# Performance work log

Hardware: AMD Instinct MI355X
Metric: run time of the kernel (lower is better)

The kernel has to match this reference:

```python
import math
import jax, jax.numpy as jnp
import numpy as np

EPS = 1e-7
NUM_CLASSES = 13
LAMBDA_BOX, LAMBDA_OBJ, LAMBDA_CLS = 5.0, 1.0, 0.5


def setup_inputs() -> dict:
    key = jax.random.key(0)
    k0, k1, k2, kc, kcls, kox, koy, kw, kh = jax.random.split(key, 9)
    B = 32
    p0 = jax.random.normal(k0, (B, 18, 160, 160), dtype=jnp.float32)
    p1 = jax.random.normal(k1, (B, 18, 80, 80), dtype=jnp.float32)
    p2 = jax.random.normal(k2, (B, 18, 40, 40), dtype=jnp.float32)
    # Build 512 GT boxes, each in a UNIQUE cell of the coarsest (40x40) grid so the
    # scatter assignment is collision-free (matches torch's sequential loop exactly).
    N, GS = 512, 40
    cells = jax.random.permutation(kc, B * GS * GS)[:N]
    bi = cells // (GS * GS)
    rem = cells % (GS * GS)
    gj = rem // GS
    gi = rem % GS
    ox = jax.random.uniform(kox, (N,), minval=0.1, maxval=0.9)
    oy = jax.random.uniform(koy, (N,), minval=0.1, maxval=0.9)
    cx = (gi.astype(jnp.float32) + ox) / GS   # normalized 0-1
    cy = (gj.astype(jnp.float32) + oy) / GS
    w = jax.random.uniform(kw, (N,), minval=0.02, maxval=0.3)
    h = jax.random.uniform(kh, (N,), minval=0.02, maxval=0.3)
    cls = jax.random.randint(kcls, (N,), 0, NUM_CLASSES).astype(jnp.float32)
    targets = jnp.stack([bi.astype(jnp.float32), cls, cx, cy, w, h], axis=-1)
    return {"p0": p0, "p1": p1, "p2": p2, "targets": targets}


def bce_with_logits(x, t):
    # stable binary cross-entropy with logits, elementwise
    return jnp.maximum(x, 0.0) - x * t + jnp.log1p(jnp.exp(-jnp.abs(x)))


def focal_bce(pred, target, gamma=1.5, alpha=0.25):
    bce = bce_with_logits(pred, target)
    p_t = jnp.exp(-bce)
    return jnp.mean(alpha * (1.0 - p_t) ** gamma * bce)


def bbox_ciou(pred, tgt):
    # pred, tgt: (..., 4) in (cx, cy, w, h)
    pw, ph = pred[..., 2], pred[..., 3]
    tw, th = tgt[..., 2], tgt[..., 3]
    px1, px2 = pred[..., 0] - pw / 2, pred[..., 0] + pw / 2
    py1, py2 = pred[..., 1] - ph / 2, pred[..., 1] + ph / 2
    tx1, tx2 = tgt[..., 0] - tw / 2, tgt[..., 0] + tw / 2
    ty1, ty2 = tgt[..., 1] - th / 2, tgt[..., 1] + th / 2
    inter = jnp.clip(jnp.minimum(px2, tx2) - jnp.maximum(px1, tx1), 0.0) \
          * jnp.clip(jnp.minimum(py2, ty2) - jnp.maximum(py1, ty1), 0.0)
    union = pw * ph + tw * th - inter + EPS
    iou = inter / union
    ew = jnp.clip(jnp.maximum(px2, tx2) - jnp.minimum(px1, tx1), 0.0)
    eh = jnp.clip(jnp.maximum(py2, ty2) - jnp.minimum(py1, ty1), 0.0)
    c2 = ew * ew + eh * eh + EPS
    rho2 = (pred[..., 0] - tgt[..., 0]) ** 2 + (pred[..., 1] - tgt[..., 1]) ** 2
    v = (4.0 / math.pi ** 2) * (jnp.arctan(tw / (th + EPS)) - jnp.arctan(pw / (ph + EPS))) ** 2
    alpha = jax.lax.stop_gradient(v / (1.0 - iou + v + EPS))
    return iou - (rho2 / c2 + v * alpha)


def _scale_loss(pred, targets):
    # pred: (B, 5+NC, gs, gs); targets: (N, 6) [bi, cls, cx, cy, w, h] normalized
    B, C, gs, _ = pred.shape
    nc = C - 5
    bi = targets[:, 0].astype(jnp.int32)
    cls = targets[:, 1].astype(jnp.int32)
    cx, cy = targets[:, 2] * gs, targets[:, 3] * gs
    w, h = targets[:, 4] * gs, targets[:, 5] * gs
    gi = jnp.clip(jnp.floor(cx).astype(jnp.int32), 0, gs - 1)
    gj = jnp.clip(jnp.floor(cy).astype(jnp.int32), 0, gs - 1)
    obj_mask = jnp.zeros((B, gs, gs), jnp.float32).at[bi, gj, gi].set(1.0)
    tbox = jnp.zeros((B, gs, gs, 4), jnp.float32).at[bi, gj, gi].set(
        jnp.stack([cx - gi, cy - gj, w, h], axis=-1))
    tcls = jnp.zeros((B, gs, gs, nc), jnp.float32).at[bi, gj, gi, cls].set(0.95)

    p = jnp.transpose(pred, (0, 2, 3, 1))          # (B, gs, gs, C)
    p_xy = jax.nn.sigmoid(p[..., :2])
    p_wh = p[..., 2:4]
    p_obj = p[..., 4]
    p_cls = p[..., 5:]
    pbox = jnp.concatenate([p_xy, p_wh], axis=-1)  # (B, gs, gs, 4)

    iou = bbox_ciou(pbox, tbox)                    # (B, gs, gs)
    npos = jnp.sum(obj_mask)
    loss_box = jnp.sum((1.0 - iou) * obj_mask) / npos
    obj_tgt = obj_mask * jax.lax.stop_gradient(jnp.maximum(iou, 0.0))
    loss_obj = focal_bce(p_obj, obj_tgt)
    loss_cls = jnp.sum(bce_with_logits(p_cls, tcls) * obj_mask[..., None]) / (npos * nc)
    return loss_box, loss_obj, loss_cls


def reference(p0, p1, p2, targets):
    loss_box = loss_obj = loss_cls = jnp.float32(0.0)
    for pred in (p0, p1, p2):
        lb, lo, lc = _scale_loss(pred, targets)
        loss_box += lb
        loss_obj += lo
        loss_cls += lc
    total = LAMBDA_BOX * loss_box + LAMBDA_OBJ * loss_obj + LAMBDA_CLS * loss_cls
    return (total, loss_box, loss_obj, loss_cls)
```

## Files before the change

kernel.cpp:

```cpp
#include <hip/hip_runtime.h>
#include <math.h>


#define NBLK_BOX 6
#define NBLK_CLS 78
#define NBLK_TGT (NBLK_BOX + NBLK_CLS)
#define NBLK_SWEEP 525
#define NBLK_TOTAL (NBLK_TGT + NBLK_SWEEP)

namespace {
__device__ __forceinline__ float bce_logits(float x, float t) {
    return fmaxf(x, 0.0f) - x * t + log1pf(expf(-fabsf(x)));
}
__device__ __forceinline__ float focal_term(float x, float t) {
    float b = bce_logits(x, t);
    float pt = expf(-b);
    float om = fmaxf(1.0f - pt, 0.0f);
    return 0.25f * om * sqrtf(om) * b;
}
__device__ __forceinline__ float softplus_neg(float u) {
    return __logf(1.0f + __expf(u));
}
__device__ __forceinline__ float bce_fast(float x, float t) {
    return fmaxf(x, 0.0f) - x * t + softplus_neg(-fabsf(x));
}
__device__ __forceinline__ float focal0_fast(float x) {
    float b = fmaxf(x, 0.0f) + softplus_neg(-fabsf(x));
    float pt = __expf(-b);
    float om = fmaxf(1.0f - pt, 0.0f);
    return 0.25f * om * sqrtf(om) * b;
}
}

__global__ void __launch_bounds__(256) fnl_main(
    const float* __restrict__ p0, const float* __restrict__ p1,
    const float* __restrict__ p2, const float* __restrict__ tg,
    float* __restrict__ ws) {
    __shared__ float sm0[4], sm1[4];
    const float* const ps[3] = {p0, p1, p2};
    const int gss[3] = {160, 80, 40};

    float v0 = 0.0f, v1 = 0.0f;

    if (blockIdx.x < NBLK_BOX) {
        int gid = blockIdx.x * 256 + threadIdx.x;
        int s = gid >> 9;
        int t = gid & 511;

        const float bi  = tg[t * 6 + 0];
        const float cx  = tg[t * 6 + 2];
        const float cy  = tg[t * 6 + 3];
        const float w   = tg[t * 6 + 4];
        const float h   = tg[t * 6 + 5];
        const int b = (int)bi;

        const int gs = gss[s];
        const float fgs = (float)gs;
        float cxs = cx * fgs, cys = cy * fgs;
        int gi = (int)floorf(cxs); gi = min(max(gi, 0), gs - 1);
        int gj = (int)floorf(cys); gj = min(max(gj, 0), gs - 1);
        const float tx = cxs - (float)gi;
        const float ty = cys - (float)gj;
        const float tw = w * fgs;
        const float th = h * fgs;

        const int hw = gs * gs;
        const float* base = ps[s] + (size_t)b * 18 * hw + (size_t)gj * gs + gi;
        float pr0 = base[0];
        float pr1 = base[(size_t)hw];
        float pr2 = base[(size_t)2 * hw];
        float pr3 = base[(size_t)3 * hw];
        float pr4 = base[(size_t)4 * hw];

        const float px = 1.0f / (1.0f + expf(-pr0));
        const float py = 1.0f / (1.0f + expf(-pr1));
        const float pw = pr2;
        const float ph = pr3;

        const float eps = 1e-7f;
        float px1 = px - pw * 0.5f, px2 = px + pw * 0.5f;
        float py1 = py - ph * 0.5f, py2 = py + ph * 0.5f;
        float tx1 = tx - tw * 0.5f, tx2 = tx + tw * 0.5f;
        float ty1 = ty - th * 0.5f, ty2 = ty + th * 0.5f;
        float iw = fmaxf(fminf(px2, tx2) - fmaxf(px1, tx1), 0.0f);
        float ih = fmaxf(fminf(py2, ty2) - fmaxf(py1, ty1), 0.0f);
        float inter = iw * ih;
        float uni = pw * ph + tw * th - inter + eps;
        float iou = inter / uni;
        float ew = fmaxf(fmaxf(px2, tx2) - fminf(px1, tx1), 0.0f);
        float eh = fmaxf(fmaxf(py2, ty2) - fminf(py1, ty1), 0.0f);
        float c2 = ew * ew + eh * eh + eps;
        float rho2 = (px - tx) * (px - tx) + (py - ty) * (py - ty);
        const float four_over_pi2 = 0.405284734569351085775517852f;
        float dat = atanf(tw / (th + eps)) - atanf(pw / (ph + eps));
        float v = four_over_pi2 * dat * dat;
        float alpha = v / (1.0f - iou + v + eps);
        float ciou = iou - (rho2 / c2 + v * alpha);

        v0 = 1.0f - ciou;
        float tobj = fmaxf(ciou, 0.0f);
        v1 = focal_term(pr4, tobj) - focal_term(pr4, 0.0f);
    } else if (blockIdx.x < NBLK_TGT) {
        int g = (blockIdx.x - NBLK_BOX) * 256 + threadIdx.x;
        int sk = g >> 9;
        int t  = g & 511;
        int s  = sk / 13;
        int k  = sk - s * 13;

        const float bi  = tg[t * 6 + 0];
        const float clf = tg[t * 6 + 1];
        const float cx  = tg[t * 6 + 2];
        const float cy  = tg[t * 6 + 3];
        const int b = (int)bi;
        const int cls = (int)clf;

        const int gs = gss[s];
        const float fgs = (float)gs;
        int gi = (int)floorf(cx * fgs); gi = min(max(gi, 0), gs - 1);
        int gj = (int)floorf(cy * fgs); gj = min(max(gj, 0), gs - 1);

        const int hw = gs * gs;
        float x = ps[s][(size_t)b * 18 * hw + (size_t)(5 + k) * hw +
                        (size_t)gj * gs + gi];
        float tc = (k == cls) ? 0.95f : 0.0f;
        v0 = bce_fast(x, tc);
    } else {
        int chunk = blockIdx.x - NBLK_TGT;
        const float* p;
        int hw4, base4;
        if (chunk < 400)      { p = p0; hw4 = 6400; base4 = 0; }
        else if (chunk < 500) { p = p1; hw4 = 1600; base4 = 204800; }
        else                  { p = p2; hw4 = 400;  base4 = 256000; }

        int j0 = chunk * 512 + threadIdx.x - base4;
        #pragma unroll
        for (int r = 0; r < 2; ++r) {
            int idx = j0 + r * 256;
            int b = idx / hw4;
            int pos4 = idx - b * hw4;
            int hw = hw4 * 4;
            const float4* src = reinterpret_cast<const float4*>(
                p + (size_t)b * 18 * hw + (size_t)4 * hw);
            float4 x = src[pos4];
            v0 += focal0_fast(x.x) + focal0_fast(x.y) +
                  focal0_fast(x.z) + focal0_fast(x.w);
        }
    }

    for (int off = 32; off; off >>= 1) {
        v0 += __shfl_down(v0, off);
        v1 += __shfl_down(v1, off);
    }
    if ((threadIdx.x & 63) == 0) {
        sm0[threadIdx.x >> 6] = v0;
        sm1[threadIdx.x >> 6] = v1;
    }
    __syncthreads();
    if (threadIdx.x == 0) {
        ws[2 * blockIdx.x + 0] = sm0[0] + sm0[1] + sm0[2] + sm0[3];
        ws[2 * blockIdx.x + 1] = sm1[0] + sm1[1] + sm1[2] + sm1[3];
    }
}

__global__ void __launch_bounds__(256) fnl_finalize(
    const float* __restrict__ ws, float* __restrict__ out) {
    float a[12];
    #pragma unroll
    for (int j = 0; j < 12; ++j) a[j] = 0.0f;

    for (int i = threadIdx.x; i < NBLK_TOTAL; i += 256) {
        float v0 = ws[2 * i + 0];
        float v1 = ws[2 * i + 1];
        if (i < NBLK_BOX) {
            int s = i >> 1;
            a[s * 4 + 1] += v0;
            a[s * 4 + 3] += v1;
        } else if (i < NBLK_TGT) {
            int sk = (i - NBLK_BOX) >> 1;
            int s = sk / 13;
            a[s * 4 + 2] += v0;
        } else {
            int chunk = i - NBLK_TGT;
            int s = (chunk < 400) ? 0 : ((chunk < 500) ? 1 : 2);
            a[s * 4 + 0] += v0;
        }
    }

    __shared__ float red[12];
    if (threadIdx.x < 12) red[threadIdx.x] = 0.0f;
    __syncthreads();
    #pragma unroll
    for (int j = 0; j < 12; ++j) {
        float v = a[j];
        for (int off = 32; off; off >>= 1) v += __shfl_down(v, off);
        if ((threadIdx.x & 63) == 0) atomicAdd(&red[j], v);
    }
    __syncthreads();

    if (threadIdx.x == 0) {
        const float cells[3] = {819200.0f, 204800.0f, 51200.0f};
        const float npos = 512.0f;
        float lb = 0.0f, lo = 0.0f, lc = 0.0f;
        for (int s = 0; s < 3; ++s) {
            lb += red[s * 4 + 1] / npos;
            lo += (red[s * 4 + 0] + red[s * 4 + 3]) / cells[s];
            lc += red[s * 4 + 2] / (npos * 13.0f);
        }
        out[0] = 5.0f * lb + 1.0f * lo + 0.5f * lc;
        out[1] = lb;
        out[2] = lo;
        out[3] = lc;
    }
}

extern "C" void kernel_launch(void* const* d_in, const int* in_sizes, int n_in,
                              void* d_out, int out_size, void* d_ws, size_t ws_size,
                              hipStream_t stream) {
    const float* p0 = (const float*)d_in[0];
    const float* p1 = (const float*)d_in[1];
    const float* p2 = (const float*)d_in[2];
    const float* tg = (const float*)d_in[3];
    float* ws = (float*)d_ws;
    float* out = (float*)d_out;

    fnl_main<<<NBLK_TOTAL, 256, 0, stream>>>(p0, p1, p2, tg, ws);
    fnl_finalize<<<1, 256, 0, stream>>>(ws, out);
}
```

Before: 14.77 us.

## Fuse finalize into main kernel via per-block completion flags

Replaces the separate finalize launch with block 0 of the main kernel spin-waiting on per-work-block completion tags and then doing the final reduction. A small kernel that zeroes the tags runs first, so the launch count stays at two. The intent is to overlap the finalize block's launch and scheduling with the main work, at the cost of atomics, a polling loop, and reliance on forward progress of the other blocks.

```diff
diff --git a/kernel.cpp b/kernel.cpp
--- a/kernel.cpp
+++ b/kernel.cpp
@@ -6,7 +6,8 @@
 #define NBLK_CLS 78
 #define NBLK_TGT (NBLK_BOX + NBLK_CLS)
 #define NBLK_SWEEP 525
-#define NBLK_TOTAL (NBLK_TGT + NBLK_SWEEP)
+#define NWORK (NBLK_TGT + NBLK_SWEEP)
+#define TAG_OFF 2048
 
 namespace {
 __device__ __forceinline__ float bce_logits(float x, float t) {
@@ -32,18 +33,87 @@
 }
 }
 
-__global__ void __launch_bounds__(256) fnl_main(
+__global__ void fnl_zero_tags(unsigned* __restrict__ wsU) {
+    int i = threadIdx.x;
+    if (i < NWORK) wsU[TAG_OFF + i] = 0u;
+}
+
+__global__ void __launch_bounds__(256) fnl_fused(
     const float* __restrict__ p0, const float* __restrict__ p1,
     const float* __restrict__ p2, const float* __restrict__ tg,
-    float* __restrict__ ws) {
+    float* __restrict__ ws, float* __restrict__ out) {
+    unsigned* tags = reinterpret_cast<unsigned*>(ws) + TAG_OFF;
+
+    if (blockIdx.x == 0) {
+        int i0 = threadIdx.x, i1 = threadIdx.x + 256, i2 = threadIdx.x + 512;
+        bool d0 = false, d1 = (i1 >= NWORK), d2 = (i2 >= NWORK);
+        for (int it = 0; it < 1000000 && !(d0 && d1 && d2); ++it) {
+            if (!d0) d0 = (atomicAdd(&tags[i0], 0u) != 0u);
+            if (!d1) d1 = (atomicAdd(&tags[i1], 0u) != 0u);
+            if (!d2) d2 = (atomicAdd(&tags[i2], 0u) != 0u);
+            if (!(d0 && d1 && d2)) __builtin_amdgcn_s_sleep(2);
+        }
+        __syncthreads();
+
+        float a[12];
+        #pragma unroll
+        for (int j = 0; j < 12; ++j) a[j] = 0.0f;
+
+        for (int i = threadIdx.x; i < NWORK; i += 256) {
+            float v0 = atomicAdd(&ws[2 * i + 0], 0.0f);
+            float v1 = atomicAdd(&ws[2 * i + 1], 0.0f);
+            if (i < NBLK_BOX) {
+                int s = i >> 1;
+                a[s * 4 + 1] += v0;
+                a[s * 4 + 3] += v1;
+            } else if (i < NBLK_TGT) {
+                int sk = (i - NBLK_BOX) >> 1;
+                int s = sk / 13;
+                a[s * 4 + 2] += v0;
+            } else {
+                int chunk = i - NBLK_TGT;
+                int s = (chunk < 400) ? 0 : ((chunk < 500) ? 1 : 2);
+                a[s * 4 + 0] += v0;
+            }
+        }
+
+        __shared__ float red[12];
+        if (threadIdx.x < 12) red[threadIdx.x] = 0.0f;
+        __syncthreads();
+        #pragma unroll
+        for (int j = 0; j < 12; ++j) {
+            float v = a[j];
+            for (int off = 32; off; off >>= 1) v += __shfl_down(v, off);
+            if ((threadIdx.x & 63) == 0) atomicAdd(&red[j], v);
+        }
+        __syncthreads();
+
+        if (threadIdx.x == 0) {
+            const float cells[3] = {819200.0f, 204800.0f, 51200.0f};
+            const float npos = 512.0f;
+            float lb = 0.0f, lo = 0.0f, lc = 0.0f;
+            for (int s = 0; s < 3; ++s) {
+                lb += red[s * 4 + 1] / npos;
+                lo += (red[s * 4 + 0] + red[s * 4 + 3]) / cells[s];
+                lc += red[s * 4 + 2] / (npos * 13.0f);
+            }
+            out[0] = 5.0f * lb + 1.0f * lo + 0.5f * lc;
+            out[1] = lb;
+            out[2] = lo;
+            out[3] = lc;
+        }
+        return;
+    }
+
+    int wid = blockIdx.x - 1;
     __shared__ float sm0[4], sm1[4];
     const float* const ps[3] = {p0, p1, p2};
     const int gss[3] = {160, 80, 40};
 
     float v0 = 0.0f, v1 = 0.0f;
 
-    if (blockIdx.x < NBLK_BOX) {
-        int gid = blockIdx.x * 256 + threadIdx.x;
+    if (wid < NBLK_BOX) {
+        int gid = wid * 256 + threadIdx.x;
         int s = gid >> 9;
         int t = gid & 511;
 
@@ -100,8 +170,8 @@
         v0 = 1.0f - ciou;
         float tobj = fmaxf(ciou, 0.0f);
         v1 = focal_term(pr4, tobj) - focal_term(pr4, 0.0f);
-    } else if (blockIdx.x < NBLK_TGT) {
-        int g = (blockIdx.x - NBLK_BOX) * 256 + threadIdx.x;
+    } else if (wid < NBLK_TGT) {
+        int g = (wid - NBLK_BOX) * 256 + threadIdx.x;
         int sk = g >> 9;
         int t  = g & 511;
         int s  = sk / 13;
@@ -125,7 +195,7 @@
         float tc = (k == cls) ? 0.95f : 0.0f;
         v0 = bce_fast(x, tc);
     } else {
-        int chunk = blockIdx.x - NBLK_TGT;
+        int chunk = wid - NBLK_TGT;
         const float* p;
         int hw4, base4;
         if (chunk < 400)      { p = p0; hw4 = 6400; base4 = 0; }
@@ -157,59 +227,10 @@
     }
     __syncthreads();
     if (threadIdx.x == 0) {
-        ws[2 * blockIdx.x + 0] = sm0[0] + sm0[1] + sm0[2] + sm0[3];
-        ws[2 * blockIdx.x + 1] = sm1[0] + sm1[1] + sm1[2] + sm1[3];
-    }
-}
-
-__global__ void __launch_bounds__(256) fnl_finalize(
-    const float* __restrict__ ws, float* __restrict__ out) {
-    float a[12];
-    #pragma unroll
-    for (int j = 0; j < 12; ++j) a[j] = 0.0f;
-
-    for (int i = threadIdx.x; i < NBLK_TOTAL; i += 256) {
-        float v0 = ws[2 * i + 0];
-        float v1 = ws[2 * i + 1];
-        if (i < NBLK_BOX) {
-            int s = i >> 1;
-            a[s * 4 + 1] += v0;
-            a[s * 4 + 3] += v1;
-        } else if (i < NBLK_TGT) {
-            int sk = (i - NBLK_BOX) >> 1;
-            int s = sk / 13;
-            a[s * 4 + 2] += v0;
-        } else {
-            int chunk = i - NBLK_TGT;
-            int s = (chunk < 400) ? 0 : ((chunk < 500) ? 1 : 2);
-            a[s * 4 + 0] += v0;
-        }
-    }
-
-    __shared__ float red[12];
-    if (threadIdx.x < 12) red[threadIdx.x] = 0.0f;
-    __syncthreads();
-    #pragma unroll
-    for (int j = 0; j < 12; ++j) {
-        float v = a[j];
-        for (int off = 32; off; off >>= 1) v += __shfl_down(v, off);
-        if ((threadIdx.x & 63) == 0) atomicAdd(&red[j], v);
-    }
-    __syncthreads();
-
-    if (threadIdx.x == 0) {
-        const float cells[3] = {819200.0f, 204800.0f, 51200.0f};
-        const float npos = 512.0f;
-        float lb = 0.0f, lo = 0.0f, lc = 0.0f;
-        for (int s = 0; s < 3; ++s) {
-            lb += red[s * 4 + 1] / npos;
-            lo += (red[s * 4 + 0] + red[s * 4 + 3]) / cells[s];
-            lc += red[s * 4 + 2] / (npos * 13.0f);
-        }
-        out[0] = 5.0f * lb + 1.0f * lo + 0.5f * lc;
-        out[1] = lb;
-        out[2] = lo;
-        out[3] = lc;
+        atomicExch(&ws[2 * wid + 0], sm0[0] + sm0[1] + sm0[2] + sm0[3]);
+        atomicExch(&ws[2 * wid + 1], sm1[0] + sm1[1] + sm1[2] + sm1[3]);
+        asm volatile("s_waitcnt vmcnt(0)" ::: "memory");
+        atomicExch(&tags[wid], 1u);
     }
 }
 
@@ -223,6 +244,6 @@
     float* ws = (float*)d_ws;
     float* out = (float*)d_out;
 
-    fnl_main<<<NBLK_TOTAL, 256, 0, stream>>>(p0, p1, p2, tg, ws);
-    fnl_finalize<<<1, 256, 0, stream>>>(ws, out);
-}
+    fnl_zero_tags<<<1, 640, 0, stream>>>((unsigned*)d_ws);
+    fnl_fused<<<NWORK + 1, 256, 0, stream>>>(p0, p1, p2, tg, ws, out);
+}
```

New measurement: 19.33 us. +30.9%, slower.

## Fold class BCE into box blocks and enlarge objectness sweep chunks

Applied to the files above, without the earlier changes.

The class-BCE work moves from its own 78 blocks into the box blocks: each thread loads all 18 channels of its target cell and sums the 13 class terms itself. The objectness sweep for scales 0 and 1 now processes 2048 float4 per block instead of 512, cutting the grid from about 609 blocks to 156. The workspace becomes one float4 per block, so finalize can read it with a single pass and no loop. The intent is to cut block scheduling overhead and redundant target decoding, at the cost of fewer blocks for latency hiding and longer serial loads per thread in the box blocks.

```diff
diff --git a/kernel.cpp b/kernel.cpp
--- a/kernel.cpp
+++ b/kernel.cpp
@@ -3,10 +3,10 @@
 
 
 #define NBLK_BOX 6
-#define NBLK_CLS 78
-#define NBLK_TGT (NBLK_BOX + NBLK_CLS)
-#define NBLK_SWEEP 525
-#define NBLK_TOTAL (NBLK_TGT + NBLK_SWEEP)
+#define NBLK_S0 100
+#define NBLK_S1 25
+#define NBLK_S2 25
+#define NWORK (NBLK_BOX + NBLK_S0 + NBLK_S1 + NBLK_S2)
 
 namespace {
 __device__ __forceinline__ float bce_logits(float x, float t) {
@@ -35,24 +35,27 @@
 __global__ void __launch_bounds__(256) fnl_main(
     const float* __restrict__ p0, const float* __restrict__ p1,
     const float* __restrict__ p2, const float* __restrict__ tg,
-    float* __restrict__ ws) {
-    __shared__ float sm0[4], sm1[4];
-    const float* const ps[3] = {p0, p1, p2};
-    const int gss[3] = {160, 80, 40};
-
-    float v0 = 0.0f, v1 = 0.0f;
-
-    if (blockIdx.x < NBLK_BOX) {
-        int gid = blockIdx.x * 256 + threadIdx.x;
+    float4* __restrict__ ws4) {
+    __shared__ float sm0[4], sm1[4], sm2[4];
+    const int wid = blockIdx.x;
+
+    float v0 = 0.0f, v1 = 0.0f, v2 = 0.0f;
+
+    if (wid < NBLK_BOX) {
+        const float* const ps[3] = {p0, p1, p2};
+        const int gss[3] = {160, 80, 40};
+        int gid = wid * 256 + threadIdx.x;
         int s = gid >> 9;
         int t = gid & 511;
 
         const float bi  = tg[t * 6 + 0];
+        const float clf = tg[t * 6 + 1];
         const float cx  = tg[t * 6 + 2];
         const float cy  = tg[t * 6 + 3];
         const float w   = tg[t * 6 + 4];
         const float h   = tg[t * 6 + 5];
         const int b = (int)bi;
+        const int cls = (int)clf;
 
         const int gs = gss[s];
         const float fgs = (float)gs;
@@ -66,16 +69,14 @@
 
         const int hw = gs * gs;
         const float* base = ps[s] + (size_t)b * 18 * hw + (size_t)gj * gs + gi;
-        float pr0 = base[0];
-        float pr1 = base[(size_t)hw];
-        float pr2 = base[(size_t)2 * hw];
-        float pr3 = base[(size_t)3 * hw];
-        float pr4 = base[(size_t)4 * hw];
-
-        const float px = 1.0f / (1.0f + expf(-pr0));
-        const float py = 1.0f / (1.0f + expf(-pr1));
-        const float pw = pr2;
-        const float ph = pr3;
+        float pr[18];
+        #pragma unroll
+        for (int ch = 0; ch < 18; ++ch) pr[ch] = base[(size_t)ch * hw];
+
+        const float px = 1.0f / (1.0f + expf(-pr[0]));
+        const float py = 1.0f / (1.0f + expf(-pr[1]));
+        const float pw = pr[2];
+        const float ph = pr[3];
 
         const float eps = 1e-7f;
         float px1 = px - pw * 0.5f, px2 = px + pw * 0.5f;
@@ -99,42 +100,20 @@
 
         v0 = 1.0f - ciou;
         float tobj = fmaxf(ciou, 0.0f);
-        v1 = focal_term(pr4, tobj) - focal_term(pr4, 0.0f);
-    } else if (blockIdx.x < NBLK_TGT) {
-        int g = (blockIdx.x - NBLK_BOX) * 256 + threadIdx.x;
-        int sk = g >> 9;
-        int t  = g & 511;
-        int s  = sk / 13;
-        int k  = sk - s * 13;
-
-        const float bi  = tg[t * 6 + 0];
-        const float clf = tg[t * 6 + 1];
-        const float cx  = tg[t * 6 + 2];
-        const float cy  = tg[t * 6 + 3];
-        const int b = (int)bi;
-        const int cls = (int)clf;
-
-        const int gs = gss[s];
-        const float fgs = (float)gs;
-        int gi = (int)floorf(cx * fgs); gi = min(max(gi, 0), gs - 1);
-        int gj = (int)floorf(cy * fgs); gj = min(max(gj, 0), gs - 1);
-
-        const int hw = gs * gs;
-        float x = ps[s][(size_t)b * 18 * hw + (size_t)(5 + k) * hw +
-                        (size_t)gj * gs + gi];
-        float tc = (k == cls) ? 0.95f : 0.0f;
-        v0 = bce_fast(x, tc);
-    } else {
-        int chunk = blockIdx.x - NBLK_TGT;
+        v1 = focal_term(pr[4], tobj) - focal_term(pr[4], 0.0f);
+        #pragma unroll
+        for (int k = 0; k < 13; ++k) {
+            float tc = (k == cls) ? 0.95f : 0.0f;
+            v2 += bce_fast(pr[5 + k], tc);
+        }
+    } else if (wid < NBLK_BOX + NBLK_S0 + NBLK_S1) {
         const float* p;
-        int hw4, base4;
-        if (chunk < 400)      { p = p0; hw4 = 6400; base4 = 0; }
-        else if (chunk < 500) { p = p1; hw4 = 1600; base4 = 204800; }
-        else                  { p = p2; hw4 = 400;  base4 = 256000; }
-
-        int j0 = chunk * 512 + threadIdx.x - base4;
-        #pragma unroll
-        for (int r = 0; r < 2; ++r) {
+        int hw4, chunk;
+        if (wid < NBLK_BOX + NBLK_S0) { p = p0; hw4 = 6400; chunk = wid - NBLK_BOX; }
+        else                          { p = p1; hw4 = 1600; chunk = wid - NBLK_BOX - NBLK_S0; }
+        int j0 = chunk * 2048 + threadIdx.x;
+        #pragma unroll
+        for (int r = 0; r < 8; ++r) {
             int idx = j0 + r * 256;
             int b = idx / hw4;
             int pos4 = idx - b * hw4;
@@ -145,44 +124,64 @@
             v0 += focal0_fast(x.x) + focal0_fast(x.y) +
                   focal0_fast(x.z) + focal0_fast(x.w);
         }
+    } else {
+        int chunk = wid - NBLK_BOX - NBLK_S0 - NBLK_S1;
+        const int hw4 = 400, hw = 1600;
+        int j0 = chunk * 512 + threadIdx.x;
+        #pragma unroll
+        for (int r = 0; r < 2; ++r) {
+            int idx = j0 + r * 256;
+            int b = idx / hw4;
+            int pos4 = idx - b * hw4;
+            const float4* src = reinterpret_cast<const float4*>(
+                p2 + (size_t)b * 18 * hw + (size_t)4 * hw);
+            float4 x = src[pos4];
+            v0 += focal0_fast(x.x) + focal0_fast(x.y) +
+                  focal0_fast(x.z) + focal0_fast(x.w);
+        }
     }
 
     for (int off = 32; off; off >>= 1) {
         v0 += __shfl_down(v0, off);
         v1 += __shfl_down(v1, off);
+        v2 += __shfl_down(v2, off);
     }
     if ((threadIdx.x & 63) == 0) {
         sm0[threadIdx.x >> 6] = v0;
         sm1[threadIdx.x >> 6] = v1;
+        sm2[threadIdx.x >> 6] = v2;
     }
     __syncthreads();
     if (threadIdx.x == 0) {
-        ws[2 * blockIdx.x + 0] = sm0[0] + sm0[1] + sm0[2] + sm0[3];
-        ws[2 * blockIdx.x + 1] = sm1[0] + sm1[1] + sm1[2] + sm1[3];
+        float4 slot;
+        slot.x = sm0[0] + sm0[1] + sm0[2] + sm0[3];
+        slot.y = sm1[0] + sm1[1] + sm1[2] + sm1[3];
+        slot.z = sm2[0] + sm2[1] + sm2[2] + sm2[3];
+        slot.w = 0.0f;
+        ws4[wid] = slot;
     }
 }
 
 __global__ void __launch_bounds__(256) fnl_finalize(
-    const float* __restrict__ ws, float* __restrict__ out) {
+    const float4* __restrict__ ws4, float* __restrict__ out) {
     float a[12];
     #pragma unroll
     for (int j = 0; j < 12; ++j) a[j] = 0.0f;
 
-    for (int i = threadIdx.x; i < NBLK_TOTAL; i += 256) {
-        float v0 = ws[2 * i + 0];
-        float v1 = ws[2 * i + 1];
+    int i = threadIdx.x;
+    if (i < NWORK) {
+        float4 v = ws4[i];
         if (i < NBLK_BOX) {
             int s = i >> 1;
-            a[s * 4 + 1] += v0;
-            a[s * 4 + 3] += v1;
-        } else if (i < NBLK_TGT) {
-            int sk = (i - NBLK_BOX) >> 1;
-            int s = sk / 13;
-            a[s * 4 + 2] += v0;
+            a[s * 4 + 1] += v.x;
+            a[s * 4 + 3] += v.y;
+            a[s * 4 + 2] += v.z;
+        } else if (i < NBLK_BOX + NBLK_S0) {
+            a[0 * 4 + 0] += v.x;
+        } else if (i < NBLK_BOX + NBLK_S0 + NBLK_S1) {
+            a[1 * 4 + 0] += v.x;
         } else {
-            int chunk = i - NBLK_TGT;
-            int s = (chunk < 400) ? 0 : ((chunk < 500) ? 1 : 2);
-            a[s * 4 + 0] += v0;
+            a[2 * 4 + 0] += v.x;
         }
     }
 
@@ -220,9 +219,9 @@
     const float* p1 = (const float*)d_in[1];
     const float* p2 = (const float*)d_in[2];
     const float* tg = (const float*)d_in[3];
-    float* ws = (float*)d_ws;
+    float4* ws4 = (float4*)d_ws;
     float* out = (float*)d_out;
 
-    fnl_main<<<NBLK_TOTAL, 256, 0, stream>>>(p0, p1, p2, tg, ws);
-    fnl_finalize<<<1, 256, 0, stream>>>(ws, out);
-}
+    fnl_main<<<NWORK, 256, 0, stream>>>(p0, p1, p2, tg, ws4);
+    fnl_finalize<<<1, 256, 0, stream>>>(ws4, out);
+}
```

Measured after the change: 14.87 us (median of 2 runs). About the same (+0.7%).
